# Performance work log

Hardware: AMD Instinct MI355X
Metric: run time of the kernel (lower is better)

Reference implementation:

```python
import jax, jax.numpy as jnp
import numpy as np

V, R, A, C, T = 10000, 5, 8, 64, 64
EPS = 1e-3  # keras BatchNormalization default epsilon


def setup_inputs() -> dict:
    key = jax.random.key(0)
    ks = jax.random.split(key, 8)
    signal = jax.random.normal(ks[0], (V, C), dtype=jnp.float32)
    bc_idx = jax.random.randint(ks[1], (V, R, A, 3), 0, V, dtype=jnp.int32)
    bc_w = jax.random.uniform(ks[2], (V, R, A, 3), dtype=jnp.float32)
    bc_w = bc_w / jnp.sum(bc_w, axis=-1, keepdims=True)  # barycentric weights sum to 1
    scale = 0.05
    templates1 = jax.random.normal(ks[3], (T, R, A, C), dtype=jnp.float32) * scale
    bias1 = jax.random.normal(ks[4], (T,), dtype=jnp.float32) * scale
    templates2 = jax.random.normal(ks[5], (T, R, A, T), dtype=jnp.float32) * scale
    bias2 = jax.random.normal(ks[6], (T,), dtype=jnp.float32) * scale
    return {
        "signal": signal,
        "bc_w": bc_w,
        "templates1": templates1,
        "bias1": bias1,
        "gamma1": jnp.ones((T,), jnp.float32),
        "beta1": jnp.zeros((T,), jnp.float32),
        "templates2": templates2,
        "bias2": bias2,
        "gamma2": jnp.ones((T,), jnp.float32),
        "beta2": jnp.zeros((T,), jnp.float32),
        "bc_idx": bc_idx,
    }


def _conv_dirac(sig, bc_idx, bc_w, templates, bias):
    # Barycentric interpolation (the 'patch operator'): gather 3 mesh-vertex
    # signals per template point and blend. gathered: (V, R, A, 3, Cin)
    gathered = sig[bc_idx]
    interp = jnp.einsum("vraic,vrai->vrac", gathered, bc_w)  # (V, R, A, Cin)
    # All A rotations of the template along the angular axis:
    # rolled signal[a] = interp[(a - o) % A]  <=>  contract with templates[(a + o) % A].
    rot = (jnp.arange(A)[:, None] + jnp.arange(A)[None, :]) % A  # (O, A)
    t_rot = templates[:, :, rot, :]  # (T, R, O, A, Cin)
    return jnp.einsum("vrac,troac->vot", interp, t_rot) + bias  # (V, O, T)


def _angular_max_pool(x):
    # Pick, per vertex, the rotation with maximal Euclidean response norm.
    idx = jnp.argmax(jnp.linalg.norm(x, axis=-1), axis=1)  # (V,)
    return jnp.take_along_axis(x, idx[:, None, None], axis=1)[:, 0, :]  # (V, T)


def _bn_inference(x, gamma, beta):
    # Fresh BN at inference: moving_mean = 0, moving_var = 1.
    inv = jax.lax.rsqrt(jnp.asarray(1.0 + EPS, x.dtype))
    return gamma * (x * inv) + beta


def reference(signal, bc_w, templates1, bias1, gamma1, beta1,
              templates2, bias2, gamma2, beta2, bc_idx):
    s = _conv_dirac(signal, bc_idx, bc_w, templates1, bias1)
    s = jax.nn.relu(_bn_inference(_angular_max_pool(s), gamma1, beta1))
    s = _conv_dirac(s, bc_idx, bc_w, templates2, bias2)
    s = _bn_inference(_angular_max_pool(s), gamma2, beta2)
    # input_dim == amt_templates -> identity shortcut (no rescale branch)
    return jax.nn.relu(s + signal)
```

## Files before the change

kernel.cpp:

```cpp
#include <hip/hip_runtime.h>

#define NVV 10000
#define NKSTEPS 80
#define KSPLIT 40
#define BN_INV 0.99950037468777316f

#define AS1 __attribute__((address_space(1)))
#define AS3 __attribute__((address_space(3)))

typedef float f32x4 __attribute__((ext_vector_type(4)));
typedef short short8 __attribute__((ext_vector_type(8)));
typedef unsigned short ushort;

#define ACH_USH 5120
#define ACH_B   10240
#define WCH_B   16384

__device__ __forceinline__ ushort bsplit(float v, float& rem) {
    unsigned u = __float_as_uint(v);
    unsigned r = (u + 0x7fffu + ((u >> 16) & 1u)) & 0xffff0000u;
    rem = v - __uint_as_float(r);
    return (ushort)(r >> 16);
}

__device__ __forceinline__ void interp_store2(ushort* __restrict__ dstp, int it,
                                              const float4& g0, const float4& g1, const float4& g2,
                                              float w0, float w1, float w2) {
    const int m = it >> 3, kq = it & 7;
    const float av[4] = {g0.x, g0.y, g0.z, g0.w};
    const float bv[4] = {g1.x, g1.y, g1.z, g1.w};
    const float cv[4] = {g2.x, g2.y, g2.z, g2.w};
    ushort h1[4], h2[4];
    #pragma unroll
    for (int e = 0; e < 4; ++e) {
        const float vv = w0 * av[e] + w1 * bv[e] + w2 * cv[e];
        float r1, r2;
        h1[e] = bsplit(vv, r1); h2[e] = bsplit(r1, r2);
    }
    const int mt = m >> 4, mm = m & 15, qk = kq >> 1, hf = kq & 1;
    const int o0 = ((mt * 2 + 0) * 4 + qk) * 128 + mm * 8 + hf * 4;
    *(uint2*)(dstp + o0)       = make_uint2((unsigned)h1[0] | ((unsigned)h1[1] << 16),
                                            (unsigned)h1[2] | ((unsigned)h1[3] << 16));
    *(uint2*)(dstp + o0 + 512) = make_uint2((unsigned)h2[0] | ((unsigned)h2[1] << 16),
                                            (unsigned)h2[2] | ((unsigned)h2[3] << 16));
}

__global__ void build_w_kernel(const float* __restrict__ t1,
                               const float* __restrict__ t2,
                               ushort* __restrict__ W1g,
                               ushort* __restrict__ W2g) {
    const int k = blockIdx.x;
    const int n = threadIdx.x;
    const float* T  = blockIdx.y ? t2 : t1;
    ushort*      Wg = blockIdx.y ? W2g : W1g;
    const int r = k >> 9, a = (k >> 6) & 7, c = k & 63;
    const int o = n >> 6, t = n & 63;
    const float w = T[((t * 5 + r) * 8 + ((o + a) & 7)) * 64 + c];
    float r1, r2;
    const ushort h1 = bsplit(w, r1);
    const ushort h2 = bsplit(r1, r2);
    const int kstep = k >> 5, kw = k & 31, q = kw >> 3, kk = kw & 7;
    const int strip = n >> 7, nl = n & 127, nt = nl >> 4, l16 = nl & 15;
    const size_t base = (size_t)(kstep * 4 + strip) * 8192;
    const int off = ((nt * 2 + 0) * 4 + q) * 128 + l16 * 8 + kk;
    Wg[base + off]       = h1;
    Wg[base + off + 512] = h2;
}

__global__ void interp_kernel(const float* __restrict__ src,
                              const int*   __restrict__ bc_idx,
                              const float* __restrict__ bc_w,
                              ushort*      __restrict__ Ag,
                              int mg0) {
    const int cid = blockIdx.x;
    const int mgl = cid / NKSTEPS;
    const int ks  = cid % NKSTEPS;
    const int mg  = mg0 + mgl;
    const int x   = threadIdx.x;
    ushort* chunk = Ag + (size_t)cid * ACH_USH;
    const int ra = ks >> 1;
    #pragma unroll
    for (int s = 0; s < 3; ++s) {
        const int it = x + 256 * s;
        if (it < 640) {
            const int m = it >> 3, kq = it & 7;
            const int v = mg * 80 + m;
            const int*   ip = bc_idx + v * 120 + ra * 3;
            const float* wp = bc_w  + v * 120 + ra * 3;
            const int c0 = (ks & 1) * 32 + kq * 4;
            const float4 g0 = *(const float4*)(src + (size_t)ip[0] * 64 + c0);
            const float4 g1 = *(const float4*)(src + (size_t)ip[1] * 64 + c0);
            const float4 g2 = *(const float4*)(src + (size_t)ip[2] * 64 + c0);
            interp_store2(chunk, it, g0, g1, g2, wp[0], wp[1], wp[2]);
        }
    }
}

#define GEMM_LOADS(AB, WB, KS)                                              \
    if ((KS) < ksend) {                                                     \
        const AS1 char* an = aBase + (size_t)(KS) * ACH_B;                  \
        const AS1 char* wn = wBase + (size_t)(KS) * (4 * WCH_B);            \
        _Pragma("unroll")                                                   \
        for (int f = 0; f < 10; ++f)                                        \
            AB[f] = *(const AS1 short8*)(an + f * 1024);                    \
        _Pragma("unroll")                                                   \
        for (int f = 0; f < 16; ++f)                                        \
            WB[f] = *(const AS1 short8*)(wn + f * 1024);                    \
    }

#define GEMM_MFMAS(AB, WB)                                                  \
    _Pragma("unroll")                                                       \
    for (int mt = 0; mt < 5; ++mt) {                                        \
        _Pragma("unroll")                                                   \
        for (int nt = 0; nt < 8; ++nt) {                                    \
            d[mt][nt] = __builtin_amdgcn_mfma_f32_16x16x32_bf16(            \
                AB[mt * 2 + 0], WB[nt * 2 + 0], d[mt][nt], 0, 0, 0);        \
            d[mt][nt] = __builtin_amdgcn_mfma_f32_16x16x32_bf16(            \
                AB[mt * 2 + 0], WB[nt * 2 + 1], d[mt][nt], 0, 0, 0);        \
            d[mt][nt] = __builtin_amdgcn_mfma_f32_16x16x32_bf16(            \
                AB[mt * 2 + 1], WB[nt * 2 + 0], d[mt][nt], 0, 0, 0);        \
        }                                                                   \
    }

__global__ __launch_bounds__(256, 1)
void gemm_kernel(const ushort* __restrict__ Ag,
                 const ushort* __restrict__ Wg,
                 float*       __restrict__ S1,
                 float*       __restrict__ S2,
                 int mg0) {
    const int b = blockIdx.x;
    const int mgl   = b >> 1;
    const int khalf = b & 1;
    const int Mbase = (mg0 + mgl) * 80;
    const int x = threadIdx.x;
    const int wj   = x >> 6;
    const int lane = x & 63;
    const int l16  = lane & 15;
    const int q    = lane >> 4;
    const int ks0   = khalf * KSPLIT;
    const int ksend = ks0 + KSPLIT;

    f32x4 d[5][8] = {};

    const AS1 char* aBase = (const AS1 char*)Ag
        + (size_t)mgl * NKSTEPS * ACH_B + lane * 16;
    const AS1 char* wBase = (const AS1 char*)Wg
        + (size_t)wj * WCH_B + lane * 16;

    short8 A0[10], W0[16], A1[10], W1[16];

    GEMM_LOADS(A0, W0, ks0);

    for (int ks = ks0; ks < ksend; ks += 2) {
        GEMM_LOADS(A1, W1, ks + 1);
        GEMM_MFMAS(A0, W0);
        GEMM_LOADS(A0, W0, ks + 2);
        GEMM_MFMAS(A1, W1);
    }

    float* Sh = khalf ? S2 : S1;
    #pragma unroll
    for (int mt = 0; mt < 5; ++mt) {
        #pragma unroll
        for (int nt = 0; nt < 8; ++nt) {
            #pragma unroll
            for (int r = 0; r < 4; ++r) {
                const int mglob = Mbase + mt * 16 + q * 4 + r;
                const int nglob = wj * 128 + nt * 16 + l16;
                Sh[(size_t)mglob * 512 + nglob] = d[mt][nt][r];
            }
        }
    }
}

template<bool RES>
__global__ void pool_kernel(const float* __restrict__ S1,
                            const float* __restrict__ S2,
                            const float* __restrict__ bias,
                            const float* __restrict__ gamma,
                            const float* __restrict__ beta,
                            const float* __restrict__ resid,
                            float*       __restrict__ dst) {
    const int w = threadIdx.x >> 6;
    const int t = threadIdx.x & 63;
    const int v = blockIdx.x * 4 + w;
    const float bt = bias[t];
    float vals[8], n2[8];
    #pragma unroll
    for (int o = 0; o < 8; ++o) {
        const size_t idx = (size_t)v * 512 + o * 64 + t;
        const float val = S1[idx] + S2[idx] + bt;
        vals[o] = val;
        float s = val * val;
        #pragma unroll
        for (int off = 1; off < 64; off <<= 1) s += __shfl_xor(s, off, 64);
        n2[o] = s;
    }
    int bj = 0; float bv = n2[0];
    #pragma unroll
    for (int j = 1; j < 8; ++j) {
        if (n2[j] > bv) { bv = n2[j]; bj = j; }
    }
    float val = vals[0];
    #pragma unroll
    for (int j = 1; j < 8; ++j) val = (bj == j) ? vals[j] : val;
    float r = gamma[t] * (val * BN_INV) + beta[t];
    if (RES) r += resid[(size_t)v * 64 + t];
    dst[(size_t)v * 64 + t] = fmaxf(r, 0.0f);
}

extern "C" void kernel_launch(void* const* d_in, const int* in_sizes, int n_in,
                              void* d_out, int out_size, void* d_ws, size_t ws_size,
                              hipStream_t stream) {
    const float* signal = (const float*)d_in[0];
    const float* bc_w   = (const float*)d_in[1];
    const float* t1     = (const float*)d_in[2];
    const float* bias1  = (const float*)d_in[3];
    const float* gamma1 = (const float*)d_in[4];
    const float* beta1  = (const float*)d_in[5];
    const float* t2     = (const float*)d_in[6];
    const float* bias2  = (const float*)d_in[7];
    const float* gamma2 = (const float*)d_in[8];
    const float* beta2  = (const float*)d_in[9];
    const int*   bc_idx = (const int*)d_in[10];

    const size_t WSTG = (size_t)NKSTEPS * 4 * 8192;
    ushort* W1g = (ushort*)d_ws;
    ushort* W2g = W1g + WSTG;
    float* S1 = (float*)(W2g + WSTG);
    float* S2 = S1 + (size_t)NVV * 512;
    float* s1 = S2 + (size_t)NVV * 512;
    ushort* Ag = (ushort*)(s1 + (size_t)NVV * 64);
    float* out = (float*)d_out;

    const size_t used  = (size_t)((char*)Ag - (char*)d_ws);
    const size_t avail = ws_size > used ? ws_size - used : 0;
    int P = (int)(avail / ((size_t)NKSTEPS * ACH_B));
    if (P > 125) P = 125;
    if (P < 1)  P = 1;

    build_w_kernel<<<dim3(2560, 2), 512, 0, stream>>>(t1, t2, W1g, W2g);

    for (int mg0 = 0; mg0 < 125; mg0 += P) {
        const int Pp = (125 - mg0 < P) ? (125 - mg0) : P;
        interp_kernel<<<Pp * NKSTEPS, 256, 0, stream>>>(signal, bc_idx, bc_w, Ag, mg0);
        gemm_kernel<<<2 * Pp, 256, 0, stream>>>(Ag, W1g, S1, S2, mg0);
    }
    pool_kernel<false><<<2500, 256, 0, stream>>>(S1, S2, bias1, gamma1, beta1, nullptr, s1);

    for (int mg0 = 0; mg0 < 125; mg0 += P) {
        const int Pp = (125 - mg0 < P) ? (125 - mg0) : P;
        interp_kernel<<<Pp * NKSTEPS, 256, 0, stream>>>(s1, bc_idx, bc_w, Ag, mg0);
        gemm_kernel<<<2 * Pp, 256, 0, stream>>>(Ag, W2g, S1, S2, mg0);
    }
    pool_kernel<true><<<2500, 256, 0, stream>>>(S1, S2, bias2, gamma2, beta2, signal, out);
}
```

Measured before the change: 314.3 us.

## Fuse barycentric interpolation gather into GEMM via double-buffered shared memory

Removes the separate interp kernel and its global staging buffer. Each GEMM block now gathers the three vertex rows, blends them, splits them into bf16 hi/lo, and writes the result to a double-buffered LDS tile while MFMAs run on the other buffer. This cuts the global write and read-back of the interpolated A matrix and the launch loop over chunks, at the cost of gather latency inside the GEMM and two barriers per k-step. The launch grid drops to 250 blocks covering all rows in a single pass.

```diff
diff --git a/kernel.cpp b/kernel.cpp
--- a/kernel.cpp
+++ b/kernel.cpp
@@ -6,14 +6,12 @@
 #define BN_INV 0.99950037468777316f
 
 #define AS1 __attribute__((address_space(1)))
-#define AS3 __attribute__((address_space(3)))
 
 typedef float f32x4 __attribute__((ext_vector_type(4)));
 typedef short short8 __attribute__((ext_vector_type(8)));
 typedef unsigned short ushort;
 
 #define ACH_USH 5120
-#define ACH_B   10240
 #define WCH_B   16384
 
 __device__ __forceinline__ ushort bsplit(float v, float& rem) {
@@ -67,95 +65,98 @@
     Wg[base + off + 512] = h2;
 }
 
-__global__ void interp_kernel(const float* __restrict__ src,
-                              const int*   __restrict__ bc_idx,
-                              const float* __restrict__ bc_w,
-                              ushort*      __restrict__ Ag,
-                              int mg0) {
-    const int cid = blockIdx.x;
-    const int mgl = cid / NKSTEPS;
-    const int ks  = cid % NKSTEPS;
-    const int mg  = mg0 + mgl;
-    const int x   = threadIdx.x;
-    ushort* chunk = Ag + (size_t)cid * ACH_USH;
-    const int ra = ks >> 1;
-    #pragma unroll
-    for (int s = 0; s < 3; ++s) {
-        const int it = x + 256 * s;
-        if (it < 640) {
-            const int m = it >> 3, kq = it & 7;
-            const int v = mg * 80 + m;
-            const int*   ip = bc_idx + v * 120 + ra * 3;
-            const float* wp = bc_w  + v * 120 + ra * 3;
-            const int c0 = (ks & 1) * 32 + kq * 4;
-            const float4 g0 = *(const float4*)(src + (size_t)ip[0] * 64 + c0);
-            const float4 g1 = *(const float4*)(src + (size_t)ip[1] * 64 + c0);
-            const float4 g2 = *(const float4*)(src + (size_t)ip[2] * 64 + c0);
-            interp_store2(chunk, it, g0, g1, g2, wp[0], wp[1], wp[2]);
-        }
-    }
-}
-
-#define GEMM_LOADS(AB, WB, KS)                                              \
-    if ((KS) < ksend) {                                                     \
-        const AS1 char* an = aBase + (size_t)(KS) * ACH_B;                  \
+#define GATHERS(KS)                                                         \
+    _Pragma("unroll")                                                       \
+    for (int s = 0; s < 3; ++s) {                                           \
+        const int it = x + 256 * s;                                         \
+        if (it < 640) {                                                     \
+            const int m = it >> 3, kq = it & 7;                             \
+            const int v = Mbase + m;                                        \
+            const int ra = (KS) >> 1;                                       \
+            const int*   ip = bc_idx + v * 120 + ra * 3;                    \
+            const float* wp = bc_w  + v * 120 + ra * 3;                     \
+            const int c0 = ((KS) & 1) * 32 + kq * 4;                        \
+            ga[s] = *(const float4*)(src + (size_t)ip[0] * 64 + c0);        \
+            gb[s] = *(const float4*)(src + (size_t)ip[1] * 64 + c0);        \
+            gc[s] = *(const float4*)(src + (size_t)ip[2] * 64 + c0);        \
+            wa[s] = wp[0]; wb[s] = wp[1]; wc[s] = wp[2];                    \
+        }                                                                   \
+    }
+
+#define BLENDSTORE(DST)                                                     \
+    _Pragma("unroll")                                                       \
+    for (int s = 0; s < 3; ++s) {                                           \
+        const int it = x + 256 * s;                                         \
+        if (it < 640)                                                       \
+            interp_store2((DST), it, ga[s], gb[s], gc[s], wa[s], wb[s], wc[s]); \
+    }
+
+#define WLOADS(WB, KS)                                                      \
+    {                                                                       \
         const AS1 char* wn = wBase + (size_t)(KS) * (4 * WCH_B);            \
-        _Pragma("unroll")                                                   \
-        for (int f = 0; f < 10; ++f)                                        \
-            AB[f] = *(const AS1 short8*)(an + f * 1024);                    \
         _Pragma("unroll")                                                   \
         for (int f = 0; f < 16; ++f)                                        \
             WB[f] = *(const AS1 short8*)(wn + f * 1024);                    \
     }
 
-#define GEMM_MFMAS(AB, WB)                                                  \
+#define GEMM_MFMAS(SAC, WB)                                                 \
     _Pragma("unroll")                                                       \
     for (int mt = 0; mt < 5; ++mt) {                                        \
+        const short8 a1 = *(const short8*)((SAC) + (mt * 2 + 0) * 512 + lane * 8); \
+        const short8 a2 = *(const short8*)((SAC) + (mt * 2 + 1) * 512 + lane * 8); \
         _Pragma("unroll")                                                   \
         for (int nt = 0; nt < 8; ++nt) {                                    \
             d[mt][nt] = __builtin_amdgcn_mfma_f32_16x16x32_bf16(            \
-                AB[mt * 2 + 0], WB[nt * 2 + 0], d[mt][nt], 0, 0, 0);        \
+                a1, WB[nt * 2 + 0], d[mt][nt], 0, 0, 0);                    \
             d[mt][nt] = __builtin_amdgcn_mfma_f32_16x16x32_bf16(            \
-                AB[mt * 2 + 0], WB[nt * 2 + 1], d[mt][nt], 0, 0, 0);        \
+                a1, WB[nt * 2 + 1], d[mt][nt], 0, 0, 0);                    \
             d[mt][nt] = __builtin_amdgcn_mfma_f32_16x16x32_bf16(            \
-                AB[mt * 2 + 1], WB[nt * 2 + 0], d[mt][nt], 0, 0, 0);        \
+                a2, WB[nt * 2 + 0], d[mt][nt], 0, 0, 0);                    \
         }                                                                   \
     }
 
 __global__ __launch_bounds__(256, 1)
-void gemm_kernel(const ushort* __restrict__ Ag,
+void gemm_kernel(const float* __restrict__ src,
+                 const int*   __restrict__ bc_idx,
+                 const float* __restrict__ bc_w,
                  const ushort* __restrict__ Wg,
                  float*       __restrict__ S1,
-                 float*       __restrict__ S2,
-                 int mg0) {
+                 float*       __restrict__ S2) {
+    __shared__ ushort sA[2][ACH_USH];
     const int b = blockIdx.x;
     const int mgl   = b >> 1;
     const int khalf = b & 1;
-    const int Mbase = (mg0 + mgl) * 80;
+    const int Mbase = mgl * 80;
+    const int ks0   = khalf * KSPLIT;
+    const int ksend = ks0 + KSPLIT;
     const int x = threadIdx.x;
     const int wj   = x >> 6;
     const int lane = x & 63;
     const int l16  = lane & 15;
     const int q    = lane >> 4;
-    const int ks0   = khalf * KSPLIT;
-    const int ksend = ks0 + KSPLIT;
 
     f32x4 d[5][8] = {};
 
-    const AS1 char* aBase = (const AS1 char*)Ag
-        + (size_t)mgl * NKSTEPS * ACH_B + lane * 16;
-    const AS1 char* wBase = (const AS1 char*)Wg
-        + (size_t)wj * WCH_B + lane * 16;
-
-    short8 A0[10], W0[16], A1[10], W1[16];
-
-    GEMM_LOADS(A0, W0, ks0);
+    const AS1 char* wBase = (const AS1 char*)Wg + (size_t)wj * WCH_B + lane * 16;
+
+    short8 W0[16], W1[16];
+    float4 ga[3], gb[3], gc[3];
+    float  wa[3], wb[3], wc[3];
+
+    WLOADS(W0, ks0);
+    GATHERS(ks0);
+    BLENDSTORE(sA[0]);
+    __syncthreads();
 
     for (int ks = ks0; ks < ksend; ks += 2) {
-        GEMM_LOADS(A1, W1, ks + 1);
-        GEMM_MFMAS(A0, W0);
-        GEMM_LOADS(A0, W0, ks + 2);
-        GEMM_MFMAS(A1, W1);
+        if (ks + 1 < ksend) { WLOADS(W1, ks + 1); GATHERS(ks + 1); }
+        GEMM_MFMAS(sA[0], W0);
+        if (ks + 1 < ksend) BLENDSTORE(sA[1]);
+        __syncthreads();
+        if (ks + 2 < ksend) { WLOADS(W0, ks + 2); GATHERS(ks + 2); }
+        GEMM_MFMAS(sA[1], W1);
+        if (ks + 2 < ksend) BLENDSTORE(sA[0]);
+        __syncthreads();
     }
 
     float* Sh = khalf ? S2 : S1;
@@ -230,28 +231,13 @@
     float* S1 = (float*)(W2g + WSTG);
     float* S2 = S1 + (size_t)NVV * 512;
     float* s1 = S2 + (size_t)NVV * 512;
-    ushort* Ag = (ushort*)(s1 + (size_t)NVV * 64);
     float* out = (float*)d_out;
 
-    const size_t used  = (size_t)((char*)Ag - (char*)d_ws);
-    const size_t avail = ws_size > used ? ws_size - used : 0;
-    int P = (int)(avail / ((size_t)NKSTEPS * ACH_B));
-    if (P > 125) P = 125;
-    if (P < 1)  P = 1;
-
     build_w_kernel<<<dim3(2560, 2), 512, 0, stream>>>(t1, t2, W1g, W2g);
 
-    for (int mg0 = 0; mg0 < 125; mg0 += P) {
-        const int Pp = (125 - mg0 < P) ? (125 - mg0) : P;
-        interp_kernel<<<Pp * NKSTEPS, 256, 0, stream>>>(signal, bc_idx, bc_w, Ag, mg0);
-        gemm_kernel<<<2 * Pp, 256, 0, stream>>>(Ag, W1g, S1, S2, mg0);
-    }
+    gemm_kernel<<<250, 256, 0, stream>>>(signal, bc_idx, bc_w, W1g, S1, S2);
     pool_kernel<false><<<2500, 256, 0, stream>>>(S1, S2, bias1, gamma1, beta1, nullptr, s1);
 
-    for (int mg0 = 0; mg0 < 125; mg0 += P) {
-        const int Pp = (125 - mg0 < P) ? (125 - mg0) : P;
-        interp_kernel<<<Pp * NKSTEPS, 256, 0, stream>>>(s1, bc_idx, bc_w, Ag, mg0);
-        gemm_kernel<<<2 * Pp, 256, 0, stream>>>(Ag, W2g, S1, S2, mg0);
-    }
+    gemm_kernel<<<250, 256, 0, stream>>>(s1, bc_idx, bc_w, W2g, S1, S2);
     pool_kernel<true><<<2500, 256, 0, stream>>>(S1, S2, bias2, gamma2, beta2, signal, out);
 }
```

Result: slower. 418.9 us (+33.3%).
